# Performance work log

Measured on AMD Instinct MI355X. Metric: run time of the kernel, lower is better.

The kernel has to match this reference:

```python
import jax, jax.numpy as jnp
import numpy as np

RADIUS = [1.0, 1.5, 2.0, 100.0]  # bucket boundaries; last is catch-all
NFILT = len(RADIUS)
C_IN, C_OUT = 256, 512


def setup_inputs() -> dict:
    key = jax.random.key(0)
    k1, k2, k3, k4 = jax.random.split(key, 4)
    b, n = 16, 4096
    feat = jax.random.normal(k1, (b, n, C_IN), dtype=jnp.float32)
    xyz = jax.random.normal(k2, (b, n, 3), dtype=jnp.float32)
    # init per original reset_parameters
    std = 2.0 * np.sqrt(2.0 / (C_IN + C_OUT))
    a = np.sqrt(3.0) * std
    weight = jax.random.uniform(k3, (NFILT, C_OUT, C_IN), dtype=jnp.float32, minval=-a, maxval=a)
    bound = 1.0 / np.sqrt(C_IN)
    bias = jax.random.uniform(k4, (NFILT, C_OUT), dtype=jnp.float32, minval=-bound, maxval=bound)
    return {"feat": feat, "xyz": xyz, "weight": weight, "bias": bias}


def reference(feat, xyz, weight, bias):
    b, n, c = feat.shape
    p = feat.reshape(b * n, c)                      # (P, C)
    radii = jnp.asarray(RADIUS, dtype=feat.dtype)
    r_norm = jnp.linalg.norm(xyz.reshape(b * n, 3), axis=1)
    # first radius with r_norm < r (same as the sequential break in map2filtId)
    filt_id = jnp.argmax(r_norm[:, None] < radii[None, :], axis=1)  # (P,)
    # grouped linear expressed densely: all Nfilt GEMMs, then per-point select
    all_out = jnp.einsum('pc,foc->fpo', p, weight) + bias[:, None, :]  # (F, P, O)
    out = jnp.take_along_axis(all_out, filt_id[None, :, None], axis=0)[0]  # (P, O)
    return out.reshape(b, n, -1)
```

## Files before the change

kernel.cpp:

```cpp
#include <hip/hip_runtime.h>
#include <hip/hip_bf16.h>

#define C_IN   256
#define C_OUT  512
#define NFILT  4

#define BM 128
#define BN 128
#define BK 32
#define SAS 40

#define NSTEP 8

typedef __attribute__((ext_vector_type(8))) short bf16x8;
typedef __attribute__((ext_vector_type(4))) float floatx4;

union Pack8 { uint4 u; __hip_bfloat16 h[8]; };

__global__ __launch_bounds__(1024) void bucketize_kernel(
    const float* __restrict__ xyz, int* __restrict__ idxbuf,
    int* __restrict__ cnt, int P)
{
    __shared__ int hist[NFILT];
    __shared__ int wbase[16][NFILT];
    __shared__ int gbase[NFILT];

    int tid = threadIdx.x;
    int wid = tid >> 6;
    int lane = tid & 63;
    if (tid < NFILT) hist[tid] = 0;
    __syncthreads();

    int pid = blockIdx.x * 1024 + tid;
    int filt = -1;
    if (pid < P) {
        float x = xyz[pid * 3 + 0];
        float y = xyz[pid * 3 + 1];
        float z = xyz[pid * 3 + 2];
        float r2 = __fadd_rn(__fadd_rn(__fmul_rn(x, x), __fmul_rn(y, y)), __fmul_rn(z, z));
        float r = sqrtf(r2);
        if (r < 1.0f)        filt = 0;
        else if (r < 1.5f)   filt = 1;
        else if (r < 2.0f)   filt = 2;
        else if (r < 100.0f) filt = 3;
        else                 filt = 0;
    }

    int myoff = 0;
#pragma unroll
    for (int f = 0; f < NFILT; ++f) {
        unsigned long long m = __ballot(filt == f);
        if (lane == 0) wbase[wid][f] = atomicAdd(&hist[f], (int)__popcll(m));
        if (filt == f) myoff = __popcll(m & ((1ull << lane) - 1ull));
    }
    __syncthreads();
    if (tid < NFILT) gbase[tid] = atomicAdd(&cnt[tid], hist[tid]);
    __syncthreads();

    if (filt >= 0)
        idxbuf[filt * P + gbase[filt] + wbase[wid][filt] + myoff] = pid;
}

__global__ void convert_w_kernel(const float* __restrict__ w,
                                 ushort* __restrict__ wb,
                                 int* __restrict__ cnt) {
    if (blockIdx.x == 0 && threadIdx.x < NFILT) cnt[threadIdx.x] = 0;
    int i = (blockIdx.x * blockDim.x + threadIdx.x) * 4;
    float4 v = *(const float4*)(w + i);
    union { ushort4 u; __hip_bfloat16 h[4]; } cv;
    cv.h[0] = __float2bfloat16(v.x);
    cv.h[1] = __float2bfloat16(v.y);
    cv.h[2] = __float2bfloat16(v.z);
    cv.h[3] = __float2bfloat16(v.w);
    *(ushort4*)(wb + i) = cv.u;
}

__global__ __launch_bounds__(256) void gather_kernel(
    const float* __restrict__ feat, const int* __restrict__ idxbuf,
    const int* __restrict__ cnt, ushort* __restrict__ gA, int P)
{
    int wid = threadIdx.x >> 6;
    int lane = threadIdx.x & 63;
    int slot = blockIdx.x * 4 + wid;
    if (slot >= P) return;
    int c0 = cnt[0], c1 = cnt[1], c2 = cnt[2];
    int b1 = c0, b2 = c0 + c1, b3 = c0 + c1 + c2;
    int f, i;
    if (slot < b1)      { f = 0; i = slot; }
    else if (slot < b2) { f = 1; i = slot - b1; }
    else if (slot < b3) { f = 2; i = slot - b2; }
    else                { f = 3; i = slot - b3; }
    int pid = idxbuf[f * P + i];
    float4 v = *(const float4*)(feat + (size_t)pid * C_IN + lane * 4);
    union { ushort4 u; __hip_bfloat16 h[4]; } cv;
    cv.h[0] = __float2bfloat16(v.x);
    cv.h[1] = __float2bfloat16(v.y);
    cv.h[2] = __float2bfloat16(v.z);
    cv.h[3] = __float2bfloat16(v.w);
    *(ushort4*)(gA + (size_t)slot * C_IN + lane * 4) = cv.u;
}

#define STAGE32(s, b) do {                                                      \
    int kByte = (s) * 64;                                                       \
    _Pragma("unroll")                                                           \
    for (int n = 0; n < 2; ++n) {                                               \
        int seg = wid * 2 + n;                             \
        int row = seg * 16 + (lane >> 2);                                       \
        const char* srcA = aBase + ((size_t)(gBase + row) * (C_IN * 2))         \
                                 + kByte + schunk * 16;                         \
        __builtin_amdgcn_global_load_lds(                                       \
            (const __attribute__((address_space(1))) void*)srcA,                \
            (__attribute__((address_space(3))) void*)&sA[b][seg * 512], 16, 0, 0); \
        const char* srcB = bBase + ((size_t)(wRow0 + row) * (C_IN * 2))         \
                                 + kByte + schunk * 16;                         \
        __builtin_amdgcn_global_load_lds(                                       \
            (const __attribute__((address_space(1))) void*)srcB,                \
            (__attribute__((address_space(3))) void*)&sB[b][seg * 512], 16, 0, 0); \
    }                                                                           \
} while (0)

__global__ __launch_bounds__(256, 4) void gemm_fast_kernel(
    const ushort* __restrict__ gA, const ushort* __restrict__ wb,
    const float* __restrict__ bias, const int* __restrict__ idxbuf,
    const int* __restrict__ cnt, float* __restrict__ out, int P)
{
    __shared__ ushort sA[2][BM * 32];
    __shared__ ushort sB[2][BN * 32];
    __shared__ int    sIdx[BM];
    __shared__ float  sBias[BN];

    int lid = blockIdx.x + (blockIdx.y << 2);
    int g = lid & 7;
    int q = lid >> 3;
    int cTile = q & 3;
    int t = ((q >> 2) << 3) + g;

    int c0 = cnt[0], c1 = cnt[1], c2 = cnt[2], c3 = cnt[3];
    int counts[4] = {c0, c1, c2, c3};
    int bases[4]  = {0, c0, c0 + c1, c0 + c1 + c2};
    int f = -1, lt = 0;
    for (int ff = 0; ff < 4; ++ff) {
        int nt = (counts[ff] + BM - 1) / BM;
        if (t < nt) { f = ff; lt = t; break; }
        t -= nt;
    }
    if (f < 0) return;

    int tid = threadIdx.x;
    int oBase = cTile * BN;
    int cn = counts[f];
    int gBase = bases[f] + lt * BM;
    int wRow0 = f * C_OUT + oBase;

    int wid = tid >> 6;
    int lane = tid & 63;
    int wm = (wid >> 1) * 64;
    int wn = (wid & 1) * 64;
    int lcol = lane & 15;
    int quad = lane >> 4;

    int rchunk = (quad ^ ((lcol >> 1) & 3)) * 8;

    int schunk = (lane & 3) ^ ((lane >> 3) & 3);

    const char* aBase = (const char*)gA;
    const char* bBase = (const char*)wb;

    STAGE32(0, 0);
    if (tid < BM) {
        int r = lt * BM + tid;
        sIdx[tid] = (r < cn) ? idxbuf[f * P + r] : -1;
    }
    if (tid < BN) sBias[tid] = bias[f * C_OUT + oBase + tid];
    __syncthreads();

    floatx4 acc[4][4];
#pragma unroll
    for (int i = 0; i < 4; ++i)
#pragma unroll
        for (int j = 0; j < 4; ++j)
            acc[i][j] = (floatx4){0.f, 0.f, 0.f, 0.f};

#pragma unroll
    for (int s = 0; s < NSTEP; ++s) {
        if (s < NSTEP - 1) STAGE32(s + 1, (s + 1) & 1);
        __builtin_amdgcn_sched_barrier(0);

        const ushort* cA = sA[s & 1];
        const ushort* cB = sB[s & 1];
        bf16x8 af[4], bfr[4];
#pragma unroll
        for (int i = 0; i < 4; ++i)
            af[i] = *(const bf16x8*)&cA[(wm + i * 16 + lcol) * 32 + rchunk];
#pragma unroll
        for (int j = 0; j < 4; ++j)
            bfr[j] = *(const bf16x8*)&cB[(wn + j * 16 + lcol) * 32 + rchunk];
#pragma unroll
        for (int i = 0; i < 4; ++i)
#pragma unroll
            for (int j = 0; j < 4; ++j)
                acc[i][j] = __builtin_amdgcn_mfma_f32_16x16x32_bf16(af[i], bfr[j], acc[i][j], 0, 0, 0);

        asm volatile("s_waitcnt vmcnt(0)" ::: "memory");
        __builtin_amdgcn_s_barrier();
        __builtin_amdgcn_sched_barrier(0);
    }

#pragma unroll
    for (int i = 0; i < 4; ++i) {
        int r0 = wm + i * 16 + quad * 4;
        int pid0 = sIdx[r0 + 0];
        int pid1 = sIdx[r0 + 1];
        int pid2 = sIdx[r0 + 2];
        int pid3 = sIdx[r0 + 3];
#pragma unroll
        for (int j = 0; j < 4; ++j) {
            int o = oBase + wn + j * 16 + lcol;
            float bv = sBias[wn + j * 16 + lcol];
            if (pid0 >= 0) out[pid0 * C_OUT + o] = acc[i][j][0] + bv;
            if (pid1 >= 0) out[pid1 * C_OUT + o] = acc[i][j][1] + bv;
            if (pid2 >= 0) out[pid2 * C_OUT + o] = acc[i][j][2] + bv;
            if (pid3 >= 0) out[pid3 * C_OUT + o] = acc[i][j][3] + bv;
        }
    }
}

__global__ __launch_bounds__(256) void gemm_kernel(
    const float* __restrict__ feat, const ushort* __restrict__ wb,
    const float* __restrict__ bias, const int* __restrict__ idxbuf,
    const int* __restrict__ cnt, float* __restrict__ out, int P)
{
    __shared__ ushort sA[BM * SAS];
    __shared__ ushort sB[BN * SAS];
    __shared__ int    sIdx[BM];
    __shared__ float  sBias[BN];

    int lid = blockIdx.x + (blockIdx.y << 2);
    int g = lid & 7;
    int q = lid >> 3;
    int cTile = q & 3;
    int t = ((q >> 2) << 3) + g;

    int counts[4];
    counts[0] = cnt[0]; counts[1] = cnt[1]; counts[2] = cnt[2]; counts[3] = cnt[3];
    int f = -1, lt = 0;
    for (int ff = 0; ff < 4; ++ff) {
        int nt = (counts[ff] + BM - 1) / BM;
        if (t < nt) { f = ff; lt = t; break; }
        t -= nt;
    }
    if (f < 0) return;

    int tid = threadIdx.x;
    int oBase = cTile * BN;
    int rowBase = lt * BM;
    int cn = counts[f];

    if (tid < BM) {
        int r = rowBase + tid;
        sIdx[tid] = (r < cn) ? idxbuf[f * P + r] : -1;
    }
    if (tid < BN) sBias[tid] = bias[f * C_OUT + oBase + tid];
    __syncthreads();

    int sRow = tid >> 1;
    int sHalf = tid & 1;
    int myIdx = sIdx[sRow];
    const float* aRow = feat + (size_t)(myIdx < 0 ? 0 : myIdx) * C_IN + sHalf * 16;
    const ushort* bRow = wb + (size_t)(f * C_OUT + oBase + sRow) * C_IN + sHalf * 16;

    int wid = tid >> 6;
    int lane = tid & 63;
    int wm = (wid >> 1) * 64;
    int wn = (wid & 1) * 64;
    int lcol = lane & 15;
    int quad = lane >> 4;

    floatx4 acc[4][4];
#pragma unroll
    for (int i = 0; i < 4; ++i)
#pragma unroll
        for (int j = 0; j < 4; ++j)
            acc[i][j] = (floatx4){0.f, 0.f, 0.f, 0.f};

    for (int kk = 0; kk < C_IN; kk += BK) {
        const float* ap = aRow + kk;
        float4 a0 = *(const float4*)(ap + 0);
        float4 a1 = *(const float4*)(ap + 4);
        float4 a2 = *(const float4*)(ap + 8);
        float4 a3 = *(const float4*)(ap + 12);
        const ushort* bp = bRow + kk;
        uint4 b01 = *(const uint4*)(bp + 0);
        uint4 b23 = *(const uint4*)(bp + 8);

        Pack8 p0, p1;
        p0.h[0] = __float2bfloat16(a0.x); p0.h[1] = __float2bfloat16(a0.y);
        p0.h[2] = __float2bfloat16(a0.z); p0.h[3] = __float2bfloat16(a0.w);
        p0.h[4] = __float2bfloat16(a1.x); p0.h[5] = __float2bfloat16(a1.y);
        p0.h[6] = __float2bfloat16(a1.z); p0.h[7] = __float2bfloat16(a1.w);
        p1.h[0] = __float2bfloat16(a2.x); p1.h[1] = __float2bfloat16(a2.y);
        p1.h[2] = __float2bfloat16(a2.z); p1.h[3] = __float2bfloat16(a2.w);
        p1.h[4] = __float2bfloat16(a3.x); p1.h[5] = __float2bfloat16(a3.y);
        p1.h[6] = __float2bfloat16(a3.z); p1.h[7] = __float2bfloat16(a3.w);

        ushort* dA = &sA[sRow * SAS + sHalf * 16];
        *(uint4*)(dA + 0) = p0.u;
        *(uint4*)(dA + 8) = p1.u;
        ushort* dB = &sB[sRow * SAS + sHalf * 16];
        *(uint4*)(dB + 0) = b01;
        *(uint4*)(dB + 8) = b23;

        __syncthreads();

        bf16x8 af[4], bfr[4];
#pragma unroll
        for (int i = 0; i < 4; ++i)
            af[i] = *(const bf16x8*)&sA[(wm + i * 16 + lcol) * SAS + quad * 8];
#pragma unroll
        for (int j = 0; j < 4; ++j)
            bfr[j] = *(const bf16x8*)&sB[(wn + j * 16 + lcol) * SAS + quad * 8];
#pragma unroll
        for (int i = 0; i < 4; ++i)
#pragma unroll
            for (int j = 0; j < 4; ++j)
                acc[i][j] = __builtin_amdgcn_mfma_f32_16x16x32_bf16(af[i], bfr[j], acc[i][j], 0, 0, 0);

        __syncthreads();
    }

#pragma unroll
    for (int i = 0; i < 4; ++i) {
        int r0 = wm + i * 16 + quad * 4;
        int pid0 = sIdx[r0 + 0];
        int pid1 = sIdx[r0 + 1];
        int pid2 = sIdx[r0 + 2];
        int pid3 = sIdx[r0 + 3];
#pragma unroll
        for (int j = 0; j < 4; ++j) {
            int o = oBase + wn + j * 16 + lcol;
            float bv = sBias[wn + j * 16 + lcol];
            if (pid0 >= 0) out[pid0 * C_OUT + o] = acc[i][j][0] + bv;
            if (pid1 >= 0) out[pid1 * C_OUT + o] = acc[i][j][1] + bv;
            if (pid2 >= 0) out[pid2 * C_OUT + o] = acc[i][j][2] + bv;
            if (pid3 >= 0) out[pid3 * C_OUT + o] = acc[i][j][3] + bv;
        }
    }
}

extern "C" void kernel_launch(void* const* d_in, const int* in_sizes, int n_in,
                              void* d_out, int out_size, void* d_ws, size_t ws_size,
                              hipStream_t stream) {
    const float* feat = (const float*)d_in[0];
    const float* xyz  = (const float*)d_in[1];
    const float* w    = (const float*)d_in[2];
    const float* bias = (const float*)d_in[3];
    float* out = (float*)d_out;
    int P = in_sizes[0] / C_IN;

    char* ws = (char*)d_ws;
    size_t offIdx = 0;
    size_t offCnt = (size_t)4 * P * 4;
    size_t offWb  = offCnt + 16;
    size_t offGA  = (offWb + (size_t)NFILT * C_OUT * C_IN * 2 + 255) & ~(size_t)255;
    size_t needed = offGA + (size_t)(P + BM) * C_IN * 2;

    int* idxbuf = (int*)(ws + offIdx);
    int* cntp   = (int*)(ws + offCnt);
    ushort* wb  = (ushort*)(ws + offWb);

    convert_w_kernel<<<(NFILT * C_OUT * C_IN) / 1024, 256, 0, stream>>>(w, wb, cntp);
    bucketize_kernel<<<(P + 1023) / 1024, 1024, 0, stream>>>(xyz, idxbuf, cntp, P);

    int tilesY = ((P / BM + NFILT + 7) / 8) * 8;
    dim3 grid(C_OUT / BN, tilesY);

    if (ws_size >= needed) {
        ushort* gA = (ushort*)(ws + offGA);
        gather_kernel<<<(P + 3) / 4, 256, 0, stream>>>(feat, idxbuf, cntp, gA, P);
        gemm_fast_kernel<<<grid, 256, 0, stream>>>(gA, wb, bias, idxbuf, cntp, out, P);
    } else {
        gemm_kernel<<<grid, 256, 0, stream>>>(feat, wb, bias, idxbuf, cntp, out, P);
    }
}
```

Before: 239.3 us.

## Fuse fp32 gather and bf16 conversion into GEMM with triple-buffered LDS

Drops the separate gather kernel that wrote a bf16 copy of the bucket-sorted features. The GEMM now loads fp32 feature rows straight into LDS through the per-row point index and converts them to bf16 while building fragments. The pipeline moves from two to three LDS buffers with a partial vmcnt wait, and occupancy hint drops to 2 blocks. This saves one global write and read of the gathered activations and a kernel launch, but doubles the A-tile bytes read per tile, since each A tile is reloaded in fp32 by four column blocks, and raises LDS use.

Result: no change. 239.0 us (-0.1%).

```diff
diff --git a/kernel.cpp b/kernel.cpp
--- a/kernel.cpp
+++ b/kernel.cpp
@@ -75,57 +75,37 @@
     *(ushort4*)(wb + i) = cv.u;
 }
 
-__global__ __launch_bounds__(256) void gather_kernel(
-    const float* __restrict__ feat, const int* __restrict__ idxbuf,
-    const int* __restrict__ cnt, ushort* __restrict__ gA, int P)
-{
-    int wid = threadIdx.x >> 6;
-    int lane = threadIdx.x & 63;
-    int slot = blockIdx.x * 4 + wid;
-    if (slot >= P) return;
-    int c0 = cnt[0], c1 = cnt[1], c2 = cnt[2];
-    int b1 = c0, b2 = c0 + c1, b3 = c0 + c1 + c2;
-    int f, i;
-    if (slot < b1)      { f = 0; i = slot; }
-    else if (slot < b2) { f = 1; i = slot - b1; }
-    else if (slot < b3) { f = 2; i = slot - b2; }
-    else                { f = 3; i = slot - b3; }
-    int pid = idxbuf[f * P + i];
-    float4 v = *(const float4*)(feat + (size_t)pid * C_IN + lane * 4);
-    union { ushort4 u; __hip_bfloat16 h[4]; } cv;
-    cv.h[0] = __float2bfloat16(v.x);
-    cv.h[1] = __float2bfloat16(v.y);
-    cv.h[2] = __float2bfloat16(v.z);
-    cv.h[3] = __float2bfloat16(v.w);
-    *(ushort4*)(gA + (size_t)slot * C_IN + lane * 4) = cv.u;
-}
-
-#define STAGE32(s, b) do {                                                      \
-    int kByte = (s) * 64;                                                       \
+#define STAGE_AB(s, b) do {                                                     \
+    int kByteA = (s) * 128;                                                     \
+    int kByteB = (s) * 64;                                                      \
+    _Pragma("unroll")                                                           \
+    for (int n = 0; n < 4; ++n) {                                               \
+        int seg = wid * 4 + n;                                                  \
+        const char* srcA = (const char*)feat                                    \
+            + ((size_t)sIdxv[n] * (C_IN * 4)) + kByteA + aschunk * 16;          \
+        __builtin_amdgcn_global_load_lds(                                       \
+            (const __attribute__((address_space(1))) void*)srcA,                \
+            (__attribute__((address_space(3))) void*)&sAf[b][seg * 256], 16, 0, 0); \
+    }                                                                           \
     _Pragma("unroll")                                                           \
     for (int n = 0; n < 2; ++n) {                                               \
-        int seg = wid * 2 + n;                             \
+        int seg = wid * 2 + n;                                                  \
         int row = seg * 16 + (lane >> 2);                                       \
-        const char* srcA = aBase + ((size_t)(gBase + row) * (C_IN * 2))         \
-                                 + kByte + schunk * 16;                         \
-        __builtin_amdgcn_global_load_lds(                                       \
-            (const __attribute__((address_space(1))) void*)srcA,                \
-            (__attribute__((address_space(3))) void*)&sA[b][seg * 512], 16, 0, 0); \
         const char* srcB = bBase + ((size_t)(wRow0 + row) * (C_IN * 2))         \
-                                 + kByte + schunk * 16;                         \
+                                 + kByteB + bschunk * 16;                       \
         __builtin_amdgcn_global_load_lds(                                       \
             (const __attribute__((address_space(1))) void*)srcB,                \
-            (__attribute__((address_space(3))) void*)&sB[b][seg * 512], 16, 0, 0); \
+            (__attribute__((address_space(3))) void*)&sBb[b][seg * 512], 16, 0, 0); \
     }                                                                           \
 } while (0)
 
-__global__ __launch_bounds__(256, 4) void gemm_fast_kernel(
-    const ushort* __restrict__ gA, const ushort* __restrict__ wb,
+__global__ __launch_bounds__(256, 2) void gemm_fast_kernel(
+    const float* __restrict__ feat, const ushort* __restrict__ wb,
     const float* __restrict__ bias, const int* __restrict__ idxbuf,
     const int* __restrict__ cnt, float* __restrict__ out, int P)
 {
-    __shared__ ushort sA[2][BM * 32];
-    __shared__ ushort sB[2][BN * 32];
+    __shared__ float  sAf[3][BM * 32];
+    __shared__ ushort sBb[3][BN * 32];
     __shared__ int    sIdx[BM];
     __shared__ float  sBias[BN];
 
@@ -137,7 +117,6 @@
 
     int c0 = cnt[0], c1 = cnt[1], c2 = cnt[2], c3 = cnt[3];
     int counts[4] = {c0, c1, c2, c3};
-    int bases[4]  = {0, c0, c0 + c1, c0 + c1 + c2};
     int f = -1, lt = 0;
     for (int ff = 0; ff < 4; ++ff) {
         int nt = (counts[ff] + BM - 1) / BM;
@@ -149,7 +128,6 @@
     int tid = threadIdx.x;
     int oBase = cTile * BN;
     int cn = counts[f];
-    int gBase = bases[f] + lt * BM;
     int wRow0 = f * C_OUT + oBase;
 
     int wid = tid >> 6;
@@ -159,14 +137,14 @@
     int lcol = lane & 15;
     int quad = lane >> 4;
 
-    int rchunk = (quad ^ ((lcol >> 1) & 3)) * 8;
-
-    int schunk = (lane & 3) ^ ((lane >> 3) & 3);
-
-    const char* aBase = (const char*)gA;
+    int am = lcol & 7;
+    int rchunkB = (quad ^ ((lcol >> 1) & 3)) * 8;
+
+    int aschunk = (lane & 7) ^ ((lane >> 3) & 7);
+    int bschunk = (lane & 3) ^ ((lane >> 3) & 3);
+
     const char* bBase = (const char*)wb;
 
-    STAGE32(0, 0);
     if (tid < BM) {
         int r = lt * BM + tid;
         sIdx[tid] = (r < cn) ? idxbuf[f * P + r] : -1;
@@ -174,6 +152,17 @@
     if (tid < BN) sBias[tid] = bias[f * C_OUT + oBase + tid];
     __syncthreads();
 
+    int sIdxv[4];
+#pragma unroll
+    for (int n = 0; n < 4; ++n) {
+        int r = wid * 32 + n * 8 + (lane >> 3);
+        int v = sIdx[r];
+        sIdxv[n] = (v < 0) ? 0 : v;
+    }
+
+    STAGE_AB(0, 0);
+    STAGE_AB(1, 1);
+
     floatx4 acc[4][4];
 #pragma unroll
     for (int i = 0; i < 4; ++i)
@@ -183,27 +172,39 @@
 
 #pragma unroll
     for (int s = 0; s < NSTEP; ++s) {
-        if (s < NSTEP - 1) STAGE32(s + 1, (s + 1) & 1);
+        if (s < NSTEP - 1) asm volatile("s_waitcnt vmcnt(6)" ::: "memory");
+        else               asm volatile("s_waitcnt vmcnt(0)" ::: "memory");
+        __builtin_amdgcn_s_barrier();
         __builtin_amdgcn_sched_barrier(0);
 
-        const ushort* cA = sA[s & 1];
-        const ushort* cB = sB[s & 1];
+        if (s + 2 < NSTEP) STAGE_AB(s + 2, (s + 2) % 3);
+
+        const float*  cA = sAf[s % 3];
+        const ushort* cB = sBb[s % 3];
+
         bf16x8 af[4], bfr[4];
 #pragma unroll
-        for (int i = 0; i < 4; ++i)
-            af[i] = *(const bf16x8*)&cA[(wm + i * 16 + lcol) * 32 + rchunk];
+        for (int i = 0; i < 4; ++i) {
+            int r = wm + i * 16 + lcol;
+            int p0 = (2 * quad) ^ am;
+            int p1 = (2 * quad + 1) ^ am;
+            float4 f0 = *(const float4*)&cA[r * 32 + p0 * 4];
+            float4 f1 = *(const float4*)&cA[r * 32 + p1 * 4];
+            Pack8 pk;
+            pk.h[0] = __float2bfloat16(f0.x); pk.h[1] = __float2bfloat16(f0.y);
+            pk.h[2] = __float2bfloat16(f0.z); pk.h[3] = __float2bfloat16(f0.w);
+            pk.h[4] = __float2bfloat16(f1.x); pk.h[5] = __float2bfloat16(f1.y);
+            pk.h[6] = __float2bfloat16(f1.z); pk.h[7] = __float2bfloat16(f1.w);
+            af[i] = *reinterpret_cast<bf16x8*>(&pk);
+        }
 #pragma unroll
         for (int j = 0; j < 4; ++j)
-            bfr[j] = *(const bf16x8*)&cB[(wn + j * 16 + lcol) * 32 + rchunk];
+            bfr[j] = *(const bf16x8*)&cB[(wn + j * 16 + lcol) * 32 + rchunkB];
 #pragma unroll
         for (int i = 0; i < 4; ++i)
 #pragma unroll
             for (int j = 0; j < 4; ++j)
                 acc[i][j] = __builtin_amdgcn_mfma_f32_16x16x32_bf16(af[i], bfr[j], acc[i][j], 0, 0, 0);
-
-        asm volatile("s_waitcnt vmcnt(0)" ::: "memory");
-        __builtin_amdgcn_s_barrier();
-        __builtin_amdgcn_sched_barrier(0);
     }
 
 #pragma unroll
@@ -361,8 +362,7 @@
     size_t offIdx = 0;
     size_t offCnt = (size_t)4 * P * 4;
     size_t offWb  = offCnt + 16;
-    size_t offGA  = (offWb + (size_t)NFILT * C_OUT * C_IN * 2 + 255) & ~(size_t)255;
-    size_t needed = offGA + (size_t)(P + BM) * C_IN * 2;
+    size_t needed = offWb + (size_t)NFILT * C_OUT * C_IN * 2;
 
     int* idxbuf = (int*)(ws + offIdx);
     int* cntp   = (int*)(ws + offCnt);
@@ -375,9 +375,7 @@
     dim3 grid(C_OUT / BN, tilesY);
 
     if (ws_size >= needed) {
-        ushort* gA = (ushort*)(ws + offGA);
-        gather_kernel<<<(P + 3) / 4, 256, 0, stream>>>(feat, idxbuf, cntp, gA, P);
-        gemm_fast_kernel<<<grid, 256, 0, stream>>>(gA, wb, bias, idxbuf, cntp, out, P);
+        gemm_fast_kernel<<<grid, 256, 0, stream>>>(feat, wb, bias, idxbuf, cntp, out, P);
     } else {
         gemm_kernel<<<grid, 256, 0, stream>>>(feat, wb, bias, idxbuf, cntp, out, P);
     }
```
